# Kernel tuning notes

Hardware: AMD Instinct MI355X
Metric: run time of the kernel (lower is better)

## Reference

```python
import jax, jax.numpy as jnp
import numpy as np


def setup_inputs() -> dict:
    key = jax.random.key(0)
    ks = jax.random.split(key, 9)
    B, C, H, W = 16, 512, 56, 56
    I = C // 2
    return {
        "x": jax.random.normal(ks[0], (B, C, H, W), dtype=jnp.float32),
        "g_w": jax.random.normal(ks[1], (I, C), dtype=jnp.float32) * 0.02,
        "g_b": jax.random.normal(ks[2], (I,), dtype=jnp.float32) * 0.02,
        "theta_w": jax.random.normal(ks[3], (I, C), dtype=jnp.float32) * 0.02,
        "theta_b": jax.random.normal(ks[4], (I,), dtype=jnp.float32) * 0.02,
        "phi_w": jax.random.normal(ks[5], (I, C), dtype=jnp.float32) * 0.02,
        "phi_b": jax.random.normal(ks[6], (I,), dtype=jnp.float32) * 0.02,
        "W_w": jax.random.normal(ks[7], (C, I), dtype=jnp.float32) * 0.02,
        "W_b": jax.random.normal(ks[8], (C,), dtype=jnp.float32) * 0.02,
    }


def reference(x, g_w, g_b, theta_w, theta_b, phi_w, phi_b, W_w, W_b):
    B, C, H, W = x.shape
    N = H * W
    xf = x.reshape(B, C, N)  # flatten spatial -> [B, C, N]
    # 1x1 convs == per-pixel channel matmuls
    g = jnp.einsum('ic,bcn->bin', g_w, xf) + g_b[:, None]        # [B, I, N]
    th = jnp.einsum('ic,bcn->bin', theta_w, xf) + theta_b[:, None]
    ph = jnp.einsum('ic,bcn->bin', phi_w, xf) + phi_b[:, None]
    # Original: y = (theta^T @ phi / N) @ g^T. No softmax -> reassociate:
    # y = theta^T @ ((phi @ g^T) / N), avoiding the [B, N, N] score matrix.
    M = jnp.einsum('bjn,bin->bji', ph, g) / N                    # [B, I, I]
    y = jnp.einsum('bjn,bji->bin', th, M)                        # [B, I, N]
    out = jnp.einsum('ci,bin->bcn', W_w, y) + W_b[:, None]       # [B, C, N]
    return x + out.reshape(B, C, H, W)
```

## Files before the change

kernel.cpp:

```cpp
#include <hip/hip_runtime.h>
#include <stdint.h>


typedef unsigned short ushort_t;
typedef __attribute__((ext_vector_type(8))) short short8;
typedef __attribute__((ext_vector_type(4))) float f32x4;
typedef __attribute__((ext_vector_type(4))) unsigned short us4;
typedef __attribute__((ext_vector_type(8))) unsigned short us8;

#define NSP  3136
#define XNR  3200
#define PLD  3200

#define AS1(p) ((const __attribute__((address_space(1))) void*)(p))
#define AS3(p) ((__attribute__((address_space(3))) void*)(p))

__device__ inline ushort_t f2b(float f) {
  union { float f; uint32_t u; } c; c.f = f;
  uint32_t u = c.u;
  uint32_t r = (u + 0x7fffu + ((u >> 16) & 1u)) >> 16;
  return (ushort_t)r;
}
__device__ inline float b2f(ushort_t u) {
  union { uint32_t x; float f; } c; c.x = (uint32_t)u << 16; return c.f;
}

__global__ __launch_bounds__(512, 2) void g1_8phase(
    const ushort_t* __restrict__ W2,
    const ushort_t* __restrict__ xbase,
    ushort_t* __restrict__ P,
    const float* __restrict__ bias)
{
  const int nwg = gridDim.x * gridDim.y * gridDim.z;
  int flat = blockIdx.x + gridDim.x * (blockIdx.y + gridDim.y * blockIdx.z);
  const int q = nwg >> 3;
  int swz = (flat & 7) * q + (flat >> 3);
  const int bx = swz % gridDim.x; int tmp = swz / gridDim.x;
  const int by = tmp % gridDim.y;
  const int b  = tmp / gridDim.y;

  const int m0 = bx * 256;
  const int n0 = by * 256;
  const ushort_t* Ag = W2;
  const ushort_t* Bg = xbase + (size_t)b * XNR * 512;

  const int tid = threadIdx.x;
  const int lane = tid & 63;
  const int wid = tid >> 6;
  const int wm = wid >> 2;
  const int wn = wid & 3;
  const int fr = lane & 15;
  const int fk = lane >> 4;
  const int hB = wn >> 1;
  const int rB0 = (wn & 1) * 64;
  const int s0 = ((fk) ^ (fr & 7)) * 8;
  const int s1 = ((4 | fk) ^ (fr & 7)) * 8;
  const int rth = tid >> 3;
  const int swc = ((tid & 7) ^ ((tid >> 3) & 7)) * 8;

  __shared__ __align__(16) ushort_t SM[65536];
  ushort_t (*As)[2][8192] = (ushort_t(*)[2][8192])(SM);
  ushort_t (*Bs)[2][8192] = (ushort_t(*)[2][8192])(SM + 32768);

  f32x4 acc[8][4];
#pragma unroll
  for (int i = 0; i < 8; ++i)
#pragma unroll
    for (int j = 0; j < 4; ++j) acc[i][j] = f32x4{0.f, 0.f, 0.f, 0.f};

#define STG_A(h, kt, BUF) do { \
    const ushort_t* s_ = Ag + (size_t)(m0 + (h) * 128 + rth) * 512 + (kt) * 64 + swc; \
    __builtin_amdgcn_global_load_lds(AS1(s_), AS3(&As[BUF][h][tid * 8]), 16, 0, 0); \
    __builtin_amdgcn_global_load_lds(AS1(s_ + 64 * 512), AS3(&As[BUF][h][4096 + tid * 8]), 16, 0, 0); \
  } while (0)
#define STG_B(h, kt, BUF) do { \
    const ushort_t* s_ = Bg + (size_t)(n0 + (h) * 128 + rth) * 512 + (kt) * 64 + swc; \
    __builtin_amdgcn_global_load_lds(AS1(s_), AS3(&Bs[BUF][h][tid * 8]), 16, 0, 0); \
    __builtin_amdgcn_global_load_lds(AS1(s_ + 64 * 512), AS3(&Bs[BUF][h][4096 + tid * 8]), 16, 0, 0); \
  } while (0)

#define BARR __builtin_amdgcn_s_barrier()
#define LGKM0 do { asm volatile("s_waitcnt lgkmcnt(0)" ::: "memory"); \
                   __builtin_amdgcn_sched_barrier(0); } while (0)
#define MF16(AF, BF, OFS) do { \
    __builtin_amdgcn_s_setprio(1); \
    _Pragma("unroll") for (int mf_ = 0; mf_ < 4; ++mf_) \
    _Pragma("unroll") for (int nf_ = 0; nf_ < 4; ++nf_) \
      acc[(OFS) + mf_][nf_] = __builtin_amdgcn_mfma_f32_16x16x32_bf16( \
          AF[mf_], BF[nf_], acc[(OFS) + mf_][nf_], 0, 0, 0); \
    __builtin_amdgcn_s_setprio(0); \
  } while (0)

#define TILE(T, CUR, DO_B1, DO_T2, VMN) do { \
    short8 a0[4], a1[4], a2[4], a3[4], b0[4], b1[4]; \
    _Pragma("unroll") for (int i = 0; i < 4; ++i) \
      a0[i] = *(const short8*)&As[CUR][wm][(i * 16 + fr) * 64 + s0]; \
    _Pragma("unroll") for (int i = 0; i < 4; ++i) \
      b0[i] = *(const short8*)&Bs[CUR][hB][(rB0 + i * 16 + fr) * 64 + s0]; \
    if (DO_B1) STG_B(1, (T) + 1, (CUR) ^ 1); \
    BARR; LGKM0; MF16(a0, b0, 0); BARR; \
    _Pragma("unroll") for (int i = 0; i < 4; ++i) \
      a1[i] = *(const short8*)&As[CUR][wm][((i + 4) * 16 + fr) * 64 + s0]; \
    _Pragma("unroll") for (int i = 0; i < 4; ++i) \
      b1[i] = *(const short8*)&Bs[CUR][hB][(rB0 + i * 16 + fr) * 64 + s1]; \
    BARR; LGKM0; MF16(a1, b0, 4); BARR; \
    _Pragma("unroll") for (int i = 0; i < 4; ++i) \
      a2[i] = *(const short8*)&As[CUR][wm][(i * 16 + fr) * 64 + s1]; \
    _Pragma("unroll") for (int i = 0; i < 4; ++i) \
      a3[i] = *(const short8*)&As[CUR][wm][((i + 4) * 16 + fr) * 64 + s1]; \
    if (DO_T2) STG_B(0, (T) + 2, (CUR)); \
    BARR; LGKM0; MF16(a2, b1, 0); BARR; \
    if (DO_T2) { STG_A(0, (T) + 2, (CUR)); STG_A(1, (T) + 2, (CUR)); } \
    if ((VMN) == 6) asm volatile("s_waitcnt vmcnt(6)" ::: "memory"); \
    else if ((VMN) == 0) asm volatile("s_waitcnt vmcnt(0)" ::: "memory"); \
    BARR; MF16(a3, b1, 4); BARR; \
  } while (0)

  asm volatile("s_waitcnt vmcnt(0)" ::: "memory");
  STG_A(0, 0, 0); STG_A(1, 0, 0); STG_B(0, 0, 0); STG_B(1, 0, 0);
  STG_B(0, 1, 1); STG_A(0, 1, 1); STG_A(1, 1, 1);
  asm volatile("s_waitcnt vmcnt(6)" ::: "memory");
  BARR;

  for (int t = 0; t < 6; t += 2) { TILE(t, 0, 1, 1, 6); TILE(t + 1, 1, 1, 1, 6); }
  TILE(6, 0, 1, 0, 0);
  TILE(7, 1, 0, 0, -1);

#undef TILE
#undef STG_A
#undef STG_B

  us8 z = {0, 0, 0, 0, 0, 0, 0, 0};
#pragma unroll
  for (int p = 0; p < 2; ++p) {
    if (wm == p) {
#pragma unroll
      for (int m = 0; m < 8; ++m) {
#pragma unroll
        for (int n = 0; n < 4; ++n) {
          int col = wn * 64 + n * 16 + fr;
#pragma unroll
          for (int r = 0; r < 4; ++r) {
            int lrow = m * 16 + fk * 4 + r;
            SM[lrow * 264 + col] = f2b(acc[m][n][r] + bias[m0 + p * 128 + lrow]);
          }
        }
      }
    }
    BARR;
#pragma unroll
    for (int it = 0; it < 8; ++it) {
      int idx = it * 512 + tid;
      int row = idx >> 5, ch = idx & 31;
      int gcol = n0 + ch * 8;
      if (gcol < PLD) {
        us8 v = (gcol < NSP) ? *reinterpret_cast<const us8*>(&SM[row * 264 + ch * 8]) : z;
        *reinterpret_cast<us8*>(
            &P[(size_t)b * 512 * PLD + (size_t)(m0 + p * 128 + row) * PLD + gcol]) = v;
      }
    }
    BARR;
  }
#undef BARR
#undef LGKM0
#undef MF16
}

__global__ __launch_bounds__(512, 2) void gfinal(
    const ushort_t* __restrict__ Zb,
    const ushort_t* __restrict__ xbase,
    float* __restrict__ out,
    const float* __restrict__ xres,
    const float* __restrict__ c0)
{
  const int nwg = gridDim.x * gridDim.y * gridDim.z;
  int flat = blockIdx.x + gridDim.x * (blockIdx.y + gridDim.y * blockIdx.z);
  const int q = nwg >> 3;
  int swz = (flat & 7) * q + (flat >> 3);
  const int bx = swz % gridDim.x; int tmp = swz / gridDim.x;
  const int by = tmp % gridDim.y;
  const int b  = tmp / gridDim.y;

  const int m0 = bx * 256;
  const int n0 = by * 256;
  const ushort_t* Ag = Zb + (size_t)b * 262144;
  const ushort_t* Bg = xbase + (size_t)b * XNR * 512;

  const int tid = threadIdx.x;
  const int lane = tid & 63;
  const int wid = tid >> 6;
  const int wm = wid >> 2;
  const int wn = wid & 3;
  const int fr = lane & 15;
  const int fk = lane >> 4;
  const int hB = wn >> 1;
  const int rB0 = (wn & 1) * 64;
  const int s0 = ((fk) ^ (fr & 7)) * 8;
  const int s1 = ((4 | fk) ^ (fr & 7)) * 8;
  const int rth = tid >> 3;
  const int swc = ((tid & 7) ^ ((tid >> 3) & 7)) * 8;

  __shared__ __align__(16) ushort_t SM[65536];
  ushort_t (*As)[2][8192] = (ushort_t(*)[2][8192])(SM);
  ushort_t (*Bs)[2][8192] = (ushort_t(*)[2][8192])(SM + 32768);

  f32x4 acc[8][4];
#pragma unroll
  for (int i = 0; i < 8; ++i)
#pragma unroll
    for (int j = 0; j < 4; ++j) acc[i][j] = f32x4{0.f, 0.f, 0.f, 0.f};

#define STG_A(h, kt, BUF) do { \
    const ushort_t* s_ = Ag + (size_t)(m0 + (h) * 128 + rth) * 512 + (kt) * 64 + swc; \
    __builtin_amdgcn_global_load_lds(AS1(s_), AS3(&As[BUF][h][tid * 8]), 16, 0, 0); \
    __builtin_amdgcn_global_load_lds(AS1(s_ + 64 * 512), AS3(&As[BUF][h][4096 + tid * 8]), 16, 0, 0); \
  } while (0)
#define STG_B(h, kt, BUF) do { \
    const ushort_t* s_ = Bg + (size_t)(n0 + (h) * 128 + rth) * 512 + (kt) * 64 + swc; \
    __builtin_amdgcn_global_load_lds(AS1(s_), AS3(&Bs[BUF][h][tid * 8]), 16, 0, 0); \
    __builtin_amdgcn_global_load_lds(AS1(s_ + 64 * 512), AS3(&Bs[BUF][h][4096 + tid * 8]), 16, 0, 0); \
  } while (0)

#define BARR __builtin_amdgcn_s_barrier()
#define LGKM0 do { asm volatile("s_waitcnt lgkmcnt(0)" ::: "memory"); \
                   __builtin_amdgcn_sched_barrier(0); } while (0)
#define MF16(AF, BF, OFS) do { \
    __builtin_amdgcn_s_setprio(1); \
    _Pragma("unroll") for (int mf_ = 0; mf_ < 4; ++mf_) \
    _Pragma("unroll") for (int nf_ = 0; nf_ < 4; ++nf_) \
      acc[(OFS) + mf_][nf_] = __builtin_amdgcn_mfma_f32_16x16x32_bf16( \
          AF[mf_], BF[nf_], acc[(OFS) + mf_][nf_], 0, 0, 0); \
    __builtin_amdgcn_s_setprio(0); \
  } while (0)

#define TILE(T, CUR, DO_B1, DO_T2, VMN) do { \
    short8 a0[4], a1[4], a2[4], a3[4], b0[4], b1[4]; \
    _Pragma("unroll") for (int i = 0; i < 4; ++i) \
      a0[i] = *(const short8*)&As[CUR][wm][(i * 16 + fr) * 64 + s0]; \
    _Pragma("unroll") for (int i = 0; i < 4; ++i) \
      b0[i] = *(const short8*)&Bs[CUR][hB][(rB0 + i * 16 + fr) * 64 + s0]; \
    if (DO_B1) STG_B(1, (T) + 1, (CUR) ^ 1); \
    BARR; LGKM0; MF16(a0, b0, 0); BARR; \
    _Pragma("unroll") for (int i = 0; i < 4; ++i) \
      a1[i] = *(const short8*)&As[CUR][wm][((i + 4) * 16 + fr) * 64 + s0]; \
    _Pragma("unroll") for (int i = 0; i < 4; ++i) \
      b1[i] = *(const short8*)&Bs[CUR][hB][(rB0 + i * 16 + fr) * 64 + s1]; \
    BARR; LGKM0; MF16(a1, b0, 4); BARR; \
    _Pragma("unroll") for (int i = 0; i < 4; ++i) \
      a2[i] = *(const short8*)&As[CUR][wm][(i * 16 + fr) * 64 + s1]; \
    _Pragma("unroll") for (int i = 0; i < 4; ++i) \
      a3[i] = *(const short8*)&As[CUR][wm][((i + 4) * 16 + fr) * 64 + s1]; \
    if (DO_T2) STG_B(0, (T) + 2, (CUR)); \
    BARR; LGKM0; MF16(a2, b1, 0); BARR; \
    if (DO_T2) { STG_A(0, (T) + 2, (CUR)); STG_A(1, (T) + 2, (CUR)); } \
    if ((VMN) == 6) asm volatile("s_waitcnt vmcnt(6)" ::: "memory"); \
    else if ((VMN) == 0) asm volatile("s_waitcnt vmcnt(0)" ::: "memory"); \
    BARR; MF16(a3, b1, 4); BARR; \
  } while (0)

  asm volatile("s_waitcnt vmcnt(0)" ::: "memory");
  STG_A(0, 0, 0); STG_A(1, 0, 0); STG_B(0, 0, 0); STG_B(1, 0, 0);
  STG_B(0, 1, 1); STG_A(0, 1, 1); STG_A(1, 1, 1);
  asm volatile("s_waitcnt vmcnt(6)" ::: "memory");
  BARR;

  for (int t = 0; t < 6; t += 2) { TILE(t, 0, 1, 1, 6); TILE(t + 1, 1, 1, 1, 6); }
  TILE(6, 0, 1, 0, 0);
  TILE(7, 1, 0, 0, -1);

#undef TILE
#undef STG_A
#undef STG_B

  float* SMf = (float*)SM;
  const float* c0v = c0 + (size_t)b * 512;
#pragma unroll
  for (int p = 0; p < 2; ++p) {
    if (wm == p) {
#pragma unroll
      for (int m = 0; m < 8; ++m)
#pragma unroll
        for (int n = 0; n < 4; ++n) {
          int col = wn * 64 + n * 16 + fr;
#pragma unroll
          for (int r = 0; r < 4; ++r)
            SMf[(m * 16 + fk * 4 + r) * 256 + col] = acc[m][n][r];
        }
    }
    BARR;
#pragma unroll
    for (int it = 0; it < 16; ++it) {
      int idx = it * 512 + tid;
      int row = idx >> 6, ch = idx & 63;
      int gcol = n0 + ch * 4;
      if (gcol < NSP) {
        int grow = m0 + p * 128 + row;
        size_t o = ((size_t)b * 512 + grow) * (size_t)NSP + gcol;
        f32x4 v = *reinterpret_cast<const f32x4*>(&SMf[row * 256 + ch * 4]);
        f32x4 xr = *reinterpret_cast<const f32x4*>(&xres[o]);
        float bi = c0v[grow];
        f32x4 ov = {v[0] + bi + xr[0], v[1] + bi + xr[1],
                    v[2] + bi + xr[2], v[3] + bi + xr[3]};
        *reinterpret_cast<f32x4*>(&out[o]) = ov;
      }
    }
    BARR;
  }
#undef BARR
#undef LGKM0
#undef MF16
}

template<int MODE>
__global__ __launch_bounds__(256, 2) void gemm64(
    const ushort_t* __restrict__ Abase,
    const ushort_t* __restrict__ Bbase,
    void* __restrict__ Cbase)
{
  constexpr int TB = 256;
  constexpr int MR = 4;
  constexpr int WN = 2;
  constexpr int CH = TB / 8;

  const int nwg = gridDim.x * gridDim.y * gridDim.z;
  int flat = blockIdx.x + gridDim.x * (blockIdx.y + gridDim.y * blockIdx.z);
  const int q = nwg >> 3;
  int swz = (flat & 7) * q + (flat >> 3);
  const int bx = swz % gridDim.x; int tmp = swz / gridDim.x;
  const int by = tmp % gridDim.y;
  const int bz = tmp / gridDim.y;

  int b = bz, kc = 0, kbeg = 0, kend, lda, ldb;
  const ushort_t *A, *B;
  if constexpr (MODE == 2) {
    b = bz & 15; kc = bz >> 4;
    A = Abase + (size_t)b * 512 * PLD + (size_t)256 * PLD;
    B = Abase + (size_t)b * 512 * PLD;
    lda = PLD; ldb = PLD; kbeg = kc * 640; kend = kbeg + 640;
  } else if constexpr (MODE == 6) {
    A = Abase; lda = 256;
    B = Bbase + (size_t)b * 65536; ldb = 256;
    kend = 256;
  } else {
    A = Abase + (size_t)b * 131072; lda = 256;
    B = Bbase; ldb = 256;
    kend = 256;
  }

  const int m0 = bx * 128;
  const int n0 = by * 128;
  const int tid = threadIdx.x;
  const int lane = tid & 63;
  const int wid = tid >> 6;
  const int wm = wid / WN, wn = wid % WN;
  const int fr = lane & 15;
  const int fk = lane >> 4;

  __shared__ __align__(16) ushort_t As[2][128 * 64];
  __shared__ __align__(16) ushort_t Bs[2][128 * 64];

  f32x4 acc[MR][4];
#pragma unroll
  for (int i = 0; i < MR; ++i)
#pragma unroll
    for (int j = 0; j < 4; ++j) acc[i][j] = f32x4{0.f, 0.f, 0.f, 0.f};

  const int srow = tid >> 3;
  const int lsl = (tid & 7) ^ (srow & 7);
  const ushort_t* pa = A + (size_t)(m0 + srow) * lda + kbeg + lsl * 8;
  const ushort_t* pb = B + (size_t)(n0 + srow) * ldb + kbeg + lsl * 8;

#define STAGE(bufi) do {                                                              \
    __builtin_amdgcn_global_load_lds(AS1(pa),                    AS3(&As[bufi][tid * 8]), 16, 0, 0); \
    __builtin_amdgcn_global_load_lds(AS1(pa + (size_t)CH * lda), AS3(&As[bufi][TB * 8 + tid * 8]), 16, 0, 0); \
    __builtin_amdgcn_global_load_lds(AS1(pa + (size_t)2 * CH * lda), AS3(&As[bufi][2 * TB * 8 + tid * 8]), 16, 0, 0); \
    __builtin_amdgcn_global_load_lds(AS1(pa + (size_t)3 * CH * lda), AS3(&As[bufi][3 * TB * 8 + tid * 8]), 16, 0, 0); \
    __builtin_amdgcn_global_load_lds(AS1(pb),                    AS3(&Bs[bufi][tid * 8]), 16, 0, 0); \
    __builtin_amdgcn_global_load_lds(AS1(pb + (size_t)CH * ldb), AS3(&Bs[bufi][TB * 8 + tid * 8]), 16, 0, 0); \
    __builtin_amdgcn_global_load_lds(AS1(pb + (size_t)2 * CH * ldb), AS3(&Bs[bufi][2 * TB * 8 + tid * 8]), 16, 0, 0); \
    __builtin_amdgcn_global_load_lds(AS1(pb + (size_t)3 * CH * ldb), AS3(&Bs[bufi][3 * TB * 8 + tid * 8]), 16, 0, 0); \
    pa += 64; pb += 64;                                                               \
  } while (0)

  const int sw = fr & 7;
  const int s0 = ((0 | fk) ^ sw) * 8;
  const int s1 = ((4 | fk) ^ sw) * 8;
  const int arow = (wm * MR * 16 + fr) * 64;
  const int brow = (wn * 64 + fr) * 64;

  asm volatile("s_waitcnt vmcnt(0)" ::: "memory");
  STAGE(0);

  const int nkt = (kend - kbeg) >> 6;
  for (int t = 0; t < nkt; ++t) {
    const int cur = t & 1;
    if (t + 1 < nkt) {
      STAGE(cur ^ 1);
      asm volatile("s_waitcnt vmcnt(8)" ::: "memory");
    } else {
      asm volatile("s_waitcnt vmcnt(0)" ::: "memory");
    }
    __builtin_amdgcn_s_barrier();
    __builtin_amdgcn_sched_barrier(0);

    short8 bf[4][2];
#pragma unroll
    for (int n = 0; n < 4; ++n) {
      bf[n][0] = *reinterpret_cast<const short8*>(&Bs[cur][brow + n * 1024 + s0]);
      bf[n][1] = *reinterpret_cast<const short8*>(&Bs[cur][brow + n * 1024 + s1]);
    }
    short8 af[4][2];
#pragma unroll
    for (int m = 0; m < 4; ++m) {
      af[m][0] = *reinterpret_cast<const short8*>(&As[cur][arow + m * 1024 + s0]);
      af[m][1] = *reinterpret_cast<const short8*>(&As[cur][arow + m * 1024 + s1]);
    }
    __builtin_amdgcn_s_setprio(1);
#pragma unroll
    for (int m = 0; m < 4; ++m)
#pragma unroll
      for (int n = 0; n < 4; ++n) {
        acc[m][n] = __builtin_amdgcn_mfma_f32_16x16x32_bf16(af[m][0], bf[n][0], acc[m][n], 0, 0, 0);
        acc[m][n] = __builtin_amdgcn_mfma_f32_16x16x32_bf16(af[m][1], bf[n][1], acc[m][n], 0, 0, 0);
      }
    __builtin_amdgcn_s_setprio(0);
    __builtin_amdgcn_s_barrier();
  }
#undef STAGE

  if constexpr (MODE == 2) {
    float* Mf = (float*)Cbase;
#pragma unroll
    for (int m = 0; m < MR; ++m)
#pragma unroll
      for (int n = 0; n < 4; ++n) {
        int gcol = n0 + wn * 64 + n * 16 + fr;
#pragma unroll
        for (int r = 0; r < 4; ++r) {
          int grow = m0 + wm * 64 + m * 16 + fk * 4 + r;
          Mf[((size_t)kc * 16 + b) * 65536 + grow * 256 + gcol] = acc[m][n][r];
        }
      }
  } else if constexpr (MODE == 6) {
    ushort_t* U = (ushort_t*)Cbase;
#pragma unroll
    for (int m = 0; m < MR; ++m)
#pragma unroll
      for (int n = 0; n < 4; ++n) {
        int gcol = n0 + wn * 64 + n * 16 + fr;
#pragma unroll
        for (int r = 0; r < 4; ++r) {
          int grow = m0 + wm * 64 + m * 16 + fk * 4 + r;
          U[(size_t)b * 131072 + grow * 256 + gcol] = f2b(acc[m][n][r]);
        }
      }
  } else {
    ushort_t* Z = (ushort_t*)Cbase;
#pragma unroll
    for (int m = 0; m < MR; ++m)
#pragma unroll
      for (int n = 0; n < 4; ++n) {
        int gcol = n0 + wn * 64 + n * 16 + fr;
#pragma unroll
        for (int r = 0; r < 4; ++r) {
          int grow = m0 + wm * 64 + m * 16 + fk * 4 + r;
          Z[(size_t)b * 262144 + (size_t)grow * 512 + gcol] = f2b(acc[m][n][r]);
        }
      }
  }
}

__global__ __launch_bounds__(256) void transp_x(const float* __restrict__ x,
                                                ushort_t* __restrict__ xb)
{
  const int nt = blockIdx.x, ct = blockIdx.y, b = blockIdx.z;
  const int t = threadIdx.x;
  const int n0 = nt * 64, c0 = ct * 64;
  __shared__ float Ls[64 * 65];

  if (nt == 49) {
    us8 z = {0, 0, 0, 0, 0, 0, 0, 0};
#pragma unroll
    for (int it = 0; it < 2; ++it) {
      int idx = it * 256 + t; int nl = idx >> 3, cc = idx & 7;
      *reinterpret_cast<us8*>(&xb[((size_t)b * XNR + n0 + nl) * 512 + c0 + cc * 8]) = z;
    }
    return;
  }
  const float* xs = x + (size_t)b * 512 * NSP;
#pragma unroll
  for (int p = 0; p < 4; ++p) {
    int cl = p * 16 + (t >> 4);
    int nl = (t & 15) * 4;
    f32x4 v = *reinterpret_cast<const f32x4*>(&xs[(size_t)(c0 + cl) * NSP + n0 + nl]);
    Ls[cl * 65 + nl + 0] = v[0];
    Ls[cl * 65 + nl + 1] = v[1];
    Ls[cl * 65 + nl + 2] = v[2];
    Ls[cl * 65 + nl + 3] = v[3];
  }
  __syncthreads();
#pragma unroll
  for (int it = 0; it < 2; ++it) {
    int idx = it * 256 + t; int nl = idx >> 3, cc = idx & 7;
    us8 o;
#pragma unroll
    for (int j = 0; j < 8; ++j) o[j] = f2b(Ls[(cc * 8 + j) * 65 + nl]);
    *reinterpret_cast<us8*>(&xb[((size_t)b * XNR + n0 + nl) * 512 + c0 + cc * 8]) = o;
  }
}

__global__ __launch_bounds__(256) void prep_weights(
    const float* __restrict__ g_w, const float* __restrict__ ph_w,
    const float* __restrict__ th_w, const float* __restrict__ W_w,
    const float* __restrict__ g_b, const float* __restrict__ ph_b,
    ushort_t* __restrict__ W2, ushort_t* __restrict__ TwT,
    ushort_t* __restrict__ Wwb, float* __restrict__ bias2)
{
  int i = blockIdx.x * 256 + threadIdx.x;
  if (i < 262144) {
    int row = i >> 9, col = i & 511;
    float v = (row < 256) ? g_w[row * 512 + col] : ph_w[(row - 256) * 512 + col];
    W2[i] = f2b(v);
  } else if (i < 393216) {
    int j = i - 262144; int ct = j >> 8; int k = j & 255;
    TwT[j] = f2b(th_w[(size_t)k * 512 + ct]);
  } else if (i < 524288) {
    Wwb[i - 393216] = f2b(W_w[i - 393216]);
  } else if (i < 524800) {
    int r = i - 524288;
    bias2[r] = (r < 256) ? g_b[r] : ph_b[r - 256];
  }
}

__global__ __launch_bounds__(256) void cvt_M(const float* __restrict__ Mf,
                                             ushort_t* __restrict__ MT)
{
  int i = blockIdx.x * 256 + threadIdx.x;
  const int SL = 1048576;
  float s = 0.f;
#pragma unroll
  for (int k = 0; k < 5; ++k) s += Mf[(size_t)k * SL + i];
  MT[i] = f2b(s * (1.0f / 3136.0f));
}

__global__ __launch_bounds__(256) void u3k(const ushort_t* __restrict__ U,
                                           const float* __restrict__ th_b,
                                           const float* __restrict__ W_b,
                                           float* __restrict__ c0)
{
  int i = blockIdx.x * 256 + threadIdx.x;
  int c = i & 511;
  const ushort_t* Ur = U + (size_t)i * 256;
  float a = 0.f;
#pragma unroll 4
  for (int j = 0; j < 256; ++j) a += b2f(Ur[j]) * th_b[j];
  c0[i] = a + W_b[c];
}

extern "C" void kernel_launch(void* const* d_in, const int* in_sizes, int n_in,
                              void* d_out, int out_size, void* d_ws, size_t ws_size,
                              hipStream_t stream) {
  const float* x    = (const float*)d_in[0];
  const float* g_w  = (const float*)d_in[1];
  const float* g_b  = (const float*)d_in[2];
  const float* th_w = (const float*)d_in[3];
  const float* th_b = (const float*)d_in[4];
  const float* ph_w = (const float*)d_in[5];
  const float* ph_b = (const float*)d_in[6];
  const float* W_w  = (const float*)d_in[7];
  const float* W_b  = (const float*)d_in[8];

  char* ws = (char*)d_ws;
  ushort_t* xb   = (ushort_t*)(ws + 0);
  ushort_t* P    = (ushort_t*)(ws + 52428800);
  ushort_t* U    = (ushort_t*)(ws + 52428800);
  ushort_t* Z    = (ushort_t*)(ws + 56623104);
  float*    Mf2  = (float*)(ws + 104857600);
  ushort_t* MT2  = (ushort_t*)(ws + 125829120);
  ushort_t* W2   = (ushort_t*)(ws + 127926272);
  ushort_t* TwT  = (ushort_t*)(ws + 128450560);
  ushort_t* Wwb  = (ushort_t*)(ws + 128712704);
  float*    bias2 = (float*)(ws + 128974848);
  float*    c0   = (float*)(ws + 128976896);

  prep_weights<<<2051, 256, 0, stream>>>(g_w, ph_w, th_w, W_w, g_b, ph_b,
                                         W2, TwT, Wwb, bias2);
  transp_x<<<dim3(50, 8, 16), 256, 0, stream>>>(x, xb);

  g1_8phase<<<dim3(2, 13, 16), 512, 0, stream>>>(W2, xb, P, bias2);
  gemm64<2><<<dim3(2, 2, 80), 256, 0, stream>>>(P, nullptr, Mf2);
  cvt_M<<<4096, 256, 0, stream>>>(Mf2, MT2);
  gemm64<6><<<dim3(4, 2, 16), 256, 0, stream>>>(Wwb, MT2, U);
  gemm64<7><<<dim3(4, 4, 16), 256, 0, stream>>>(U, TwT, Z);
  u3k<<<32, 256, 0, stream>>>(U, th_b, W_b, c0);
  gfinal<<<dim3(2, 13, 16), 512, 0, stream>>>(Z, xb, (float*)d_out, x, c0);
}
```

Before: 186.8 us.

## Compute theta projection in first GEMM and drop Z/bias-fold kernels

```diff
diff --git a/kernel.cpp b/kernel.cpp
--- a/kernel.cpp
+++ b/kernel.cpp
@@ -21,14 +21,12 @@
   uint32_t r = (u + 0x7fffu + ((u >> 16) & 1u)) >> 16;
   return (ushort_t)r;
 }
-__device__ inline float b2f(ushort_t u) {
-  union { uint32_t x; float f; } c; c.x = (uint32_t)u << 16; return c.f;
-}
 
 __global__ __launch_bounds__(512, 2) void g1_8phase(
-    const ushort_t* __restrict__ W2,
+    const ushort_t* __restrict__ W3,
     const ushort_t* __restrict__ xbase,
     ushort_t* __restrict__ P,
+    ushort_t* __restrict__ thT,
     const float* __restrict__ bias)
 {
   const int nwg = gridDim.x * gridDim.y * gridDim.z;
@@ -41,7 +39,7 @@
 
   const int m0 = bx * 256;
   const int n0 = by * 256;
-  const ushort_t* Ag = W2;
+  const ushort_t* Ag = W3;
   const ushort_t* Bg = xbase + (size_t)b * XNR * 512;
 
   const int tid = threadIdx.x;
@@ -130,48 +128,80 @@
 #undef STG_A
 #undef STG_B
 
-  us8 z = {0, 0, 0, 0, 0, 0, 0, 0};
-#pragma unroll
-  for (int p = 0; p < 2; ++p) {
-    if (wm == p) {
-#pragma unroll
-      for (int m = 0; m < 8; ++m) {
-#pragma unroll
-        for (int n = 0; n < 4; ++n) {
-          int col = wn * 64 + n * 16 + fr;
-#pragma unroll
-          for (int r = 0; r < 4; ++r) {
-            int lrow = m * 16 + fk * 4 + r;
-            SM[lrow * 264 + col] = f2b(acc[m][n][r] + bias[m0 + p * 128 + lrow]);
+  if (m0 == 512) {
+#pragma unroll
+    for (int p = 0; p < 2; ++p) {
+      if ((wn >> 1) == p) {
+        const int lcb = (wn & 1) * 64;
+#pragma unroll
+        for (int m = 0; m < 8; ++m) {
+          int jr = wm * 128 + m * 16 + fk * 4;
+#pragma unroll
+          for (int n = 0; n < 4; ++n) {
+            int lc = lcb + n * 16 + fr;
+            us4 o;
+#pragma unroll
+            for (int r = 0; r < 4; ++r) o[r] = f2b(acc[m][n][r] + bias[512 + jr + r]);
+            *reinterpret_cast<us4*>(&SM[lc * 264 + jr]) = o;
           }
         }
       }
-    }
-    BARR;
-#pragma unroll
-    for (int it = 0; it < 8; ++it) {
-      int idx = it * 512 + tid;
-      int row = idx >> 5, ch = idx & 31;
-      int gcol = n0 + ch * 8;
-      if (gcol < PLD) {
-        us8 v = (gcol < NSP) ? *reinterpret_cast<const us8*>(&SM[row * 264 + ch * 8]) : z;
-        *reinterpret_cast<us8*>(
-            &P[(size_t)b * 512 * PLD + (size_t)(m0 + p * 128 + row) * PLD + gcol]) = v;
-      }
-    }
-    BARR;
+      BARR;
+#pragma unroll
+      for (int it = 0; it < 8; ++it) {
+        int idx = it * 512 + tid;
+        int lc = idx >> 5, ch = idx & 31;
+        int col = n0 + p * 128 + lc;
+        if (col < NSP)
+          *reinterpret_cast<us8*>(&thT[((size_t)b * NSP + col) * 256 + ch * 8]) =
+              *reinterpret_cast<const us8*>(&SM[lc * 264 + ch * 8]);
+      }
+      BARR;
+    }
+  } else {
+    us8 z = {0, 0, 0, 0, 0, 0, 0, 0};
+#pragma unroll
+    for (int p = 0; p < 2; ++p) {
+      if (wm == p) {
+#pragma unroll
+        for (int m = 0; m < 8; ++m) {
+#pragma unroll
+          for (int n = 0; n < 4; ++n) {
+            int col = wn * 64 + n * 16 + fr;
+#pragma unroll
+            for (int r = 0; r < 4; ++r) {
+              int lrow = m * 16 + fk * 4 + r;
+              SM[lrow * 264 + col] = f2b(acc[m][n][r] + bias[m0 + p * 128 + lrow]);
+            }
+          }
+        }
+      }
+      BARR;
+#pragma unroll
+      for (int it = 0; it < 8; ++it) {
+        int idx = it * 512 + tid;
+        int row = idx >> 5, ch = idx & 31;
+        int gcol = n0 + ch * 8;
+        if (gcol < PLD) {
+          us8 v = (gcol < NSP) ? *reinterpret_cast<const us8*>(&SM[row * 264 + ch * 8]) : z;
+          *reinterpret_cast<us8*>(
+              &P[(size_t)b * 512 * PLD + (size_t)(m0 + p * 128 + row) * PLD + gcol]) = v;
+        }
+      }
+      BARR;
+    }
   }
 #undef BARR
 #undef LGKM0
 #undef MF16
 }
 
-__global__ __launch_bounds__(512, 2) void gfinal(
-    const ushort_t* __restrict__ Zb,
-    const ushort_t* __restrict__ xbase,
+__global__ __launch_bounds__(512, 2) void g4_8phase(
+    const ushort_t* __restrict__ Ub,
+    const ushort_t* __restrict__ thT,
     float* __restrict__ out,
     const float* __restrict__ xres,
-    const float* __restrict__ c0)
+    const float* __restrict__ Wb)
 {
   const int nwg = gridDim.x * gridDim.y * gridDim.z;
   int flat = blockIdx.x + gridDim.x * (blockIdx.y + gridDim.y * blockIdx.z);
@@ -183,8 +213,8 @@
 
   const int m0 = bx * 256;
   const int n0 = by * 256;
-  const ushort_t* Ag = Zb + (size_t)b * 262144;
-  const ushort_t* Bg = xbase + (size_t)b * XNR * 512;
+  const ushort_t* Ag = Ub + (size_t)b * 131072;
+  const ushort_t* Bg = thT + (size_t)b * NSP * 256;
 
   const int tid = threadIdx.x;
   const int lane = tid & 63;
@@ -211,14 +241,14 @@
     for (int j = 0; j < 4; ++j) acc[i][j] = f32x4{0.f, 0.f, 0.f, 0.f};
 
 #define STG_A(h, kt, BUF) do { \
-    const ushort_t* s_ = Ag + (size_t)(m0 + (h) * 128 + rth) * 512 + (kt) * 64 + swc; \
+    const ushort_t* s_ = Ag + (size_t)(m0 + (h) * 128 + rth) * 256 + (kt) * 64 + swc; \
     __builtin_amdgcn_global_load_lds(AS1(s_), AS3(&As[BUF][h][tid * 8]), 16, 0, 0); \
-    __builtin_amdgcn_global_load_lds(AS1(s_ + 64 * 512), AS3(&As[BUF][h][4096 + tid * 8]), 16, 0, 0); \
+    __builtin_amdgcn_global_load_lds(AS1(s_ + 64 * 256), AS3(&As[BUF][h][4096 + tid * 8]), 16, 0, 0); \
   } while (0)
 #define STG_B(h, kt, BUF) do { \
-    const ushort_t* s_ = Bg + (size_t)(n0 + (h) * 128 + rth) * 512 + (kt) * 64 + swc; \
+    const ushort_t* s_ = Bg + (size_t)(n0 + (h) * 128 + rth) * 256 + (kt) * 64 + swc; \
     __builtin_amdgcn_global_load_lds(AS1(s_), AS3(&Bs[BUF][h][tid * 8]), 16, 0, 0); \
-    __builtin_amdgcn_global_load_lds(AS1(s_ + 64 * 512), AS3(&Bs[BUF][h][4096 + tid * 8]), 16, 0, 0); \
+    __builtin_amdgcn_global_load_lds(AS1(s_ + 64 * 256), AS3(&Bs[BUF][h][4096 + tid * 8]), 16, 0, 0); \
   } while (0)
 
 #define BARR __builtin_amdgcn_s_barrier()
@@ -264,16 +294,16 @@
   asm volatile("s_waitcnt vmcnt(6)" ::: "memory");
   BARR;
 
-  for (int t = 0; t < 6; t += 2) { TILE(t, 0, 1, 1, 6); TILE(t + 1, 1, 1, 1, 6); }
-  TILE(6, 0, 1, 0, 0);
-  TILE(7, 1, 0, 0, -1);
+  TILE(0, 0, 1, 1, 6);
+  TILE(1, 1, 1, 1, 6);
+  TILE(2, 0, 1, 0, 0);
+  TILE(3, 1, 0, 0, -1);
 
 #undef TILE
 #undef STG_A
 #undef STG_B
 
   float* SMf = (float*)SM;
-  const float* c0v = c0 + (size_t)b * 512;
 #pragma unroll
   for (int p = 0; p < 2; ++p) {
     if (wm == p) {
@@ -298,7 +328,7 @@
         size_t o = ((size_t)b * 512 + grow) * (size_t)NSP + gcol;
         f32x4 v = *reinterpret_cast<const f32x4*>(&SMf[row * 256 + ch * 4]);
         f32x4 xr = *reinterpret_cast<const f32x4*>(&xres[o]);
-        float bi = c0v[grow];
+        float bi = Wb[grow];
         f32x4 ov = {v[0] + bi + xr[0], v[1] + bi + xr[1],
                     v[2] + bi + xr[2], v[3] + bi + xr[3]};
         *reinterpret_cast<f32x4*>(&out[o]) = ov;
@@ -337,13 +367,9 @@
     A = Abase + (size_t)b * 512 * PLD + (size_t)256 * PLD;
     B = Abase + (size_t)b * 512 * PLD;
     lda = PLD; ldb = PLD; kbeg = kc * 640; kend = kbeg + 640;
-  } else if constexpr (MODE == 6) {
+  } else {
     A = Abase; lda = 256;
     B = Bbase + (size_t)b * 65536; ldb = 256;
-    kend = 256;
-  } else {
-    A = Abase + (size_t)b * 131072; lda = 256;
-    B = Bbase; ldb = 256;
     kend = 256;
   }
 
@@ -441,7 +467,7 @@
           Mf[((size_t)kc * 16 + b) * 65536 + grow * 256 + gcol] = acc[m][n][r];
         }
       }
-  } else if constexpr (MODE == 6) {
+  } else {
     ushort_t* U = (ushort_t*)Cbase;
 #pragma unroll
     for (int m = 0; m < MR; ++m)
@@ -452,19 +478,6 @@
         for (int r = 0; r < 4; ++r) {
           int grow = m0 + wm * 64 + m * 16 + fk * 4 + r;
           U[(size_t)b * 131072 + grow * 256 + gcol] = f2b(acc[m][n][r]);
-        }
-      }
-  } else {
-    ushort_t* Z = (ushort_t*)Cbase;
-#pragma unroll
-    for (int m = 0; m < MR; ++m)
-#pragma unroll
-      for (int n = 0; n < 4; ++n) {
-        int gcol = n0 + wn * 64 + n * 16 + fr;
-#pragma unroll
-        for (int r = 0; r < 4; ++r) {
-          int grow = m0 + wm * 64 + m * 16 + fk * 4 + r;
-          Z[(size_t)b * 262144 + (size_t)grow * 512 + gcol] = f2b(acc[m][n][r]);
         }
       }
   }
@@ -478,15 +491,6 @@
   const int n0 = nt * 64, c0 = ct * 64;
   __shared__ float Ls[64 * 65];
 
-  if (nt == 49) {
-    us8 z = {0, 0, 0, 0, 0, 0, 0, 0};
-#pragma unroll
-    for (int it = 0; it < 2; ++it) {
-      int idx = it * 256 + t; int nl = idx >> 3, cc = idx & 7;
-      *reinterpret_cast<us8*>(&xb[((size_t)b * XNR + n0 + nl) * 512 + c0 + cc * 8]) = z;
-    }
-    return;
-  }
   const float* xs = x + (size_t)b * 512 * NSP;
 #pragma unroll
   for (int p = 0; p < 4; ++p) {
@@ -513,22 +517,22 @@
     const float* __restrict__ g_w, const float* __restrict__ ph_w,
     const float* __restrict__ th_w, const float* __restrict__ W_w,
     const float* __restrict__ g_b, const float* __restrict__ ph_b,
-    ushort_t* __restrict__ W2, ushort_t* __restrict__ TwT,
-    ushort_t* __restrict__ Wwb, float* __restrict__ bias2)
+    const float* __restrict__ th_b,
+    ushort_t* __restrict__ W3, ushort_t* __restrict__ Wwb,
+    float* __restrict__ bias3)
 {
   int i = blockIdx.x * 256 + threadIdx.x;
-  if (i < 262144) {
+  if (i < 393216) {
     int row = i >> 9, col = i & 511;
-    float v = (row < 256) ? g_w[row * 512 + col] : ph_w[(row - 256) * 512 + col];
-    W2[i] = f2b(v);
-  } else if (i < 393216) {
-    int j = i - 262144; int ct = j >> 8; int k = j & 255;
-    TwT[j] = f2b(th_w[(size_t)k * 512 + ct]);
+    float v = (row < 256) ? g_w[row * 512 + col]
+            : (row < 512) ? ph_w[(row - 256) * 512 + col]
+                          : th_w[(row - 512) * 512 + col];
+    W3[i] = f2b(v);
   } else if (i < 524288) {
     Wwb[i - 393216] = f2b(W_w[i - 393216]);
-  } else if (i < 524800) {
+  } else if (i < 525056) {
     int r = i - 524288;
-    bias2[r] = (r < 256) ? g_b[r] : ph_b[r - 256];
+    bias3[r] = (r < 256) ? g_b[r] : (r < 512) ? ph_b[r - 256] : th_b[r - 512];
   }
 }
 
@@ -541,20 +545,6 @@
 #pragma unroll
   for (int k = 0; k < 5; ++k) s += Mf[(size_t)k * SL + i];
   MT[i] = f2b(s * (1.0f / 3136.0f));
-}
-
-__global__ __launch_bounds__(256) void u3k(const ushort_t* __restrict__ U,
-                                           const float* __restrict__ th_b,
-                                           const float* __restrict__ W_b,
-                                           float* __restrict__ c0)
-{
-  int i = blockIdx.x * 256 + threadIdx.x;
-  int c = i & 511;
-  const ushort_t* Ur = U + (size_t)i * 256;
-  float a = 0.f;
-#pragma unroll 4
-  for (int j = 0; j < 256; ++j) a += b2f(Ur[j]) * th_b[j];
-  c0[i] = a + W_b[c];
 }
 
 extern "C" void kernel_launch(void* const* d_in, const int* in_sizes, int n_in,
@@ -572,26 +562,22 @@
 
   char* ws = (char*)d_ws;
   ushort_t* xb   = (ushort_t*)(ws + 0);
-  ushort_t* P    = (ushort_t*)(ws + 52428800);
-  ushort_t* U    = (ushort_t*)(ws + 52428800);
-  ushort_t* Z    = (ushort_t*)(ws + 56623104);
-  float*    Mf2  = (float*)(ws + 104857600);
-  ushort_t* MT2  = (ushort_t*)(ws + 125829120);
-  ushort_t* W2   = (ushort_t*)(ws + 127926272);
-  ushort_t* TwT  = (ushort_t*)(ws + 128450560);
-  ushort_t* Wwb  = (ushort_t*)(ws + 128712704);
-  float*    bias2 = (float*)(ws + 128974848);
-  float*    c0   = (float*)(ws + 128976896);
-
-  prep_weights<<<2051, 256, 0, stream>>>(g_w, ph_w, th_w, W_w, g_b, ph_b,
-                                         W2, TwT, Wwb, bias2);
-  transp_x<<<dim3(50, 8, 16), 256, 0, stream>>>(x, xb);
-
-  g1_8phase<<<dim3(2, 13, 16), 512, 0, stream>>>(W2, xb, P, bias2);
+  float*    Mf2  = (float*)(ws + 0);
+  ushort_t* MT2  = (ushort_t*)(ws + 41943040);
+  ushort_t* U    = (ushort_t*)(ws + 44040192);
+  ushort_t* thT  = (ushort_t*)(ws + 52428800);
+  ushort_t* P    = (ushort_t*)(ws + 78118912);
+  ushort_t* W3   = (ushort_t*)(ws + 130547712);
+  ushort_t* Wwb  = (ushort_t*)(ws + 131334144);
+  float*    bias3 = (float*)(ws + 131596288);
+
+  prep_weights<<<2052, 256, 0, stream>>>(g_w, ph_w, th_w, W_w, g_b, ph_b, th_b,
+                                         W3, Wwb, bias3);
+  transp_x<<<dim3(49, 8, 16), 256, 0, stream>>>(x, xb);
+
+  g1_8phase<<<dim3(3, 13, 16), 512, 0, stream>>>(W3, xb, P, thT, bias3);
   gemm64<2><<<dim3(2, 2, 80), 256, 0, stream>>>(P, nullptr, Mf2);
   cvt_M<<<4096, 256, 0, stream>>>(Mf2, MT2);
   gemm64<6><<<dim3(4, 2, 16), 256, 0, stream>>>(Wwb, MT2, U);
-  gemm64<7><<<dim3(4, 4, 16), 256, 0, stream>>>(U, TwT, Z);
-  u3k<<<32, 256, 0, stream>>>(U, th_b, W_b, c0);
-  gfinal<<<dim3(2, 13, 16), 512, 0, stream>>>(Z, xb, (float*)d_out, x, c0);
-}
+  g4_8phase<<<dim3(2, 13, 16), 512, 0, stream>>>(U, thT, (float*)d_out, x, W_b);
+}
```

Result: faster. 177.4 us (-5.0%).
